# Performance work log

Measured on AMD Instinct MI355X. Metric: run time of the kernel, lower is better.

Reference implementation:

```python
import jax, jax.numpy as jnp
import numpy as np

N_QUBITS = 12
N_LAYERS = 4
BATCH = 4096
DIM = 2 ** N_QUBITS  # 4096


def _apply_1q(state, U, q):
    """Apply 2x2 complex gate U to qubit q. state: (B,) + (2,)*n, wire 0 = MSB (axis q+1)."""
    state = jnp.moveaxis(state, q + 1, -1)
    state = state @ U.T
    return jnp.moveaxis(state, -1, q + 1)


def _apply_cnot(state, c, t):
    """CNOT with control c, target t: flip target amplitudes where control bit == 1."""
    flipped = jnp.flip(state, axis=t + 1)
    shape = [2 if i == c + 1 else 1 for i in range(state.ndim)]
    ctrl = jnp.arange(2).reshape(shape)
    return jnp.where(ctrl == 1, flipped, state)


def setup_inputs() -> dict:
    key = jax.random.key(0)
    k1, k2 = jax.random.split(key)
    x = jax.random.normal(k1, (BATCH, DIM), dtype=jnp.float32)
    weights = jax.random.normal(k2, (N_LAYERS, N_QUBITS, 2), dtype=jnp.float32) * 0.1
    return {"x": x, "weights": weights}


def reference(x, weights):
    n, L = N_QUBITS, N_LAYERS
    B = x.shape[0]
    # AmplitudeEmbedding with normalize=True
    norm = jnp.linalg.norm(x, axis=-1, keepdims=True)
    state = (x / norm).astype(jnp.complex64).reshape((B,) + (2,) * n)
    for layer in range(L):
        for q in range(n):
            ty = weights[layer, q, 0]
            tz = weights[layer, q, 1]
            c, s = jnp.cos(ty / 2), jnp.sin(ty / 2)
            em = jnp.exp(-0.5j * tz.astype(jnp.complex64))  # e^{-i tz/2}
            ep = jnp.exp(+0.5j * tz.astype(jnp.complex64))
            # U = RZ(tz) @ RY(ty), fused single 2x2 gate per qubit
            U = jnp.stack([
                jnp.stack([c * em, -s * em]),
                jnp.stack([s * ep, c * ep]),
            ]).astype(jnp.complex64)
            state = _apply_1q(state, U, q)
        for q in range(n - 1):
            state = _apply_cnot(state, q, q + 1)
        if n > 2:
            state = _apply_cnot(state, n - 1, 0)
    probs = jnp.abs(state) ** 2  # (B,) + (2,)*n, float32
    reduce_axes = tuple(range(1, probs.ndim))
    outs = []
    for q in range(n):
        shape = [2 if i == q + 1 else 1 for i in range(probs.ndim)]
        sign = jnp.array([1.0, -1.0], dtype=probs.dtype).reshape(shape)
        outs.append(jnp.sum(probs * sign, axis=reduce_axes))
    return jnp.stack(outs, axis=-1)  # (B, n_qubits) <Z_q> expvals
```

## Files before the change

kernel.cpp:

```cpp
#include <hip/hip_runtime.h>

#define NQ   12
#define DIM  4096
#define NL   4
#define BLK  256

typedef unsigned short u16;
typedef unsigned int   u32;

struct L12 { u16 b[NQ]; };

static constexpr u32 lap(const L12& A, u32 x){ u32 r=0; for(int p=0;p<NQ;++p) if((x>>p)&1u) r^=A.b[p]; return r; }
static constexpr L12 lcomp(const L12& A, const L12& B){ L12 r{}; for(int p=0;p<NQ;++p) r.b[p]=(u16)lap(A,(u32)B.b[p]); return r; }
static constexpr L12 lident(){ L12 r{}; for(int p=0;p<NQ;++p) r.b[p]=(u16)(1u<<p); return r; }

static constexpr u32 applyT(u32 i){
  i ^= ((i>>0)&1u) << 11;
  for(int q=10;q>=0;--q){ int pc=11-q, pt=10-q; i ^= ((i>>pc)&1u) << pt; }
  return i;
}
static constexpr L12 lT(){ L12 t{}; for(int p=0;p<NQ;++p) t.b[p]=(u16)applyT(1u<<p); return t; }

static constexpr L12 linv(const L12& A){
  u16 v[NQ]; u16 u[NQ];
  for(int p=0;p<NQ;++p){ v[p]=A.b[p]; u[p]=(u16)(1u<<p); }
  for(int t=0;t<NQ;++t){
    int p=t; while(!((v[p]>>t)&1u)) ++p;
    u16 tv=v[p]; v[p]=v[t]; v[t]=tv; u16 tu=u[p]; u[p]=u[t]; u[t]=tu;
    for(int k=0;k<NQ;++k) if(k!=t && ((v[k]>>t)&1u)){ v[k]^=v[t]; u[k]^=u[t]; }
  }
  L12 r{}; for(int p=0;p<NQ;++p) r.b[p]=u[p]; return r;
}
static constexpr L12 ltr(const L12& A){
  L12 r{}; for(int p=0;p<NQ;++p) for(int q=0;q<NQ;++q) if((A.b[p]>>q)&1u) r.b[q]=(u16)(r.b[q]|(1u<<p));
  return r;
}

struct Tables {
  u16 cm[12][16];
  u16 wg[12][4];
  u16 sp[12][4];
  u16 wexp[NQ];
};

static constexpr Tables make_tables(){
  Tables tb{};
  const L12 T   = lT();
  const L12 Tit = ltr(linv(T));
  L12 A = lident();
  L12 W = lident();
  for(int l=0;l<NL;++l){
    for(int g=0;g<3;++g){
      const int st = l*3+g;
      u16 mm[4]={0,0,0,0};
      for(int i=0;i<4;++i){ mm[i]=A.b[4*g+i]; tb.wg[st][i]=W.b[4*g+i]; }
      u32 ech[4]={0,0,0,0}; int piv[4]={0,0,0,0};
      for(int i=0;i<4;++i){
        u32 v=mm[i];
        for(int k=0;k<i;++k) if((v>>piv[k])&1u) v^=ech[k];
        int t2=11; while(!((v>>t2)&1u)) --t2;
        piv[i]=t2; ech[i]=v;
      }
      for(int a2=0;a2<4;++a2) for(int b2=a2+1;b2<4;++b2)
        if(piv[b2]<piv[a2]){ int tt=piv[a2]; piv[a2]=piv[b2]; piv[b2]=tt; }
      for(int i=0;i<4;++i) tb.sp[st][i]=(u16)piv[i];
      for(int c=0;c<16;++c){ u32 m=0; for(int i=0;i<4;++i) if((c>>i)&1) m^=mm[i]; tb.cm[st][c]=(u16)m; }
    }
    A = lcomp(A, T);
    W = lcomp(W, Tit);
  }
  for(int p=0;p<NQ;++p) tb.wexp[p]=W.b[p];
  return tb;
}

__device__ constexpr Tables TB = make_tables();

static constexpr u16 UIMG[12] = {1,2,4,8, 3,5,6,7, 9,10,11,13};

static constexpr u32 swz(u32 j){
  u32 f=0;
  for(int k=4;k<12;++k) if((j>>k)&1u) f ^= (u32)UIMG[k];
  return j ^ (f & 15u);
}

struct Derived {
  u32 lane_c[12][8];
  u32 smb[12][4];
  u32 scmb[12][16];
  u32 eps[16];
  u32 tidc[8];
  u16 esgn[12];
};

static constexpr Derived make_derived(){
  const Tables tb = make_tables();
  Derived d{};
  for(int st=0; st<12; ++st){
    bool isp[12]={false,false,false,false,false,false,false,false,false,false,false,false};
    for(int i=0;i<4;++i) isp[tb.sp[st][i]]=true;
    int np[8]; int nn=0;
    for(int p=0;p<12;++p) if(!isp[p]) np[nn++]=p;
    int best=-1;
    for(int ms=0; ms<256; ++ms){
      int pc=0; for(int k=0;k<8;++k) pc+=(ms>>k)&1;
      if(pc!=6) continue;
      u16 bas[4]={0,0,0,0}; int r=0;
      for(int k=0;k<8;++k){
        if(!((ms>>k)&1)) continue;
        u16 x=(u16)(UIMG[np[k]]&15);
        while(x){
          int hb=3; while(!((x>>hb)&1)) --hb;
          if(bas[hb]) x=(u16)(x^bas[hb]);
          else { bas[hb]=x; ++r; x=0; }
        }
      }
      if(r==4){ best=ms; break; }
    }
    if(best<0) best=0x3F;
    int pos[8]; int lo=0, hi=6;
    for(int k=0;k<8;++k){ if((best>>k)&1) pos[lo++]=np[k]; else pos[hi++]=np[k]; }
    for(int k=0;k<8;++k){
      const u32 addr = swz(1u<<pos[k])<<3;
      u32 nib=0;
      for(int i=0;i<4;++i) nib |= (u32)((tb.wg[st][i]>>pos[k])&1u)<<i;
      d.lane_c[st][k] = addr | (nib<<28);
    }
    for(int i=0;i<4;++i)  d.smb[st][i]  = swz((u32)tb.cm[st][1<<i])<<3;
    for(int c=0;c<16;++c) d.scmb[st][c] = swz((u32)tb.cm[st][c])<<3;
  }
  for(int s=0;s<16;++s) d.eps[s]  = swz((u32)s<<8)<<3;
  for(int k=0;k<8;++k)  d.tidc[k] = swz(1u<<k)<<3;
  for(int q=0;q<12;++q){
    u16 m=0;
    for(int s=0;s<16;++s){
      int par=0; u32 v=((u32)s<<8) & (u32)tb.wexp[11-q];
      while(v){ par ^= (int)(v&1u); v>>=1; }
      m |= (u16)(par<<s);
    }
    d.esgn[q]=m;
  }
  return d;
}

__device__ constexpr Derived DV = make_derived();

__device__ __forceinline__ u32 step_base(int st, int tid){
  u32 acc=0;
#pragma unroll
  for(int k=0;k<8;++k) acc ^= DV.lane_c[st][k] & (0u-((u32)(tid>>k)&1u));
  const u32 nib = acc>>28;
  u32 b = acc & 0x0FFFFFFFu;
#pragma unroll
  for(int i=0;i<4;++i) b ^= DV.smb[st][i] & (0u-((nib>>i)&1u));
  return b;
}

template<bool WITHW, bool FIRST>
__device__ __forceinline__ void do_step(int st, int tid, char* lds, const float4* gq){
  const u32 base = step_base(st, tid);
  u32 ad[16]; float ar[16], ai[16];
#pragma unroll
  for(int c=0;c<16;++c){
    ad[c] = base ^ DV.scmb[st][c];
    if(FIRST){ ar[c] = *(const float*)(lds + ad[c]); ai[c]=0.f; }
    else { const float2 v = *(const float2*)(lds + ad[c]); ar[c]=v.x; ai[c]=v.y; }
  }
#pragma unroll
  for(int i=0;i<4;++i){
    const float4 g = gq[st*4+i];
#pragma unroll
    for(int c=0;c<16;++c){
      if((c>>i)&1) continue;
      const int c1 = c | (1<<i);
      const float a0r=ar[c], a0i=ai[c], a1r=ar[c1], a1i=ai[c1];
      const float t0r = fmaf(g.x,a0r, -(g.y*a1r));
      const float t0i = fmaf(g.x,a0i, -(g.y*a1i));
      const float t1r = fmaf(g.y,a0r,  g.x*a1r);
      const float t1i = fmaf(g.y,a0i,  g.x*a1i);
      ar[c]=t0r; ai[c]=t0i;
      if(WITHW){
        ar[c1] = fmaf(g.z,t1r, -(g.w*t1i));
        ai[c1] = fmaf(g.z,t1i,  g.w*t1r);
      } else { ar[c1]=t1r; ai[c1]=t1i; }
    }
  }
#pragma unroll
  for(int c=0;c<16;++c){ float2 v; v.x=ar[c]; v.y=ai[c]; *(float2*)(lds+ad[c]) = v; }
  __syncthreads();
}

__global__ __launch_bounds__(BLK) void qsim_kernel(const float* __restrict__ x,
                                                   const float* __restrict__ w,
                                                   float* __restrict__ out)
{
  __shared__ float2 st2[DIM];
  __shared__ float4 gq[NL*NQ];
  __shared__ float  wred[4][13];
  char* lds = (char*)st2;
  const int tid = threadIdx.x;
  const int bb  = blockIdx.x;

  if (tid < NL*NQ) {
    const int l = tid/NQ, p = tid%NQ, q = (NQ-1)-p;
    const float ty = w[(l*NQ+q)*2+0];
    const float tz = w[(l*NQ+q)*2+1];
    float sy,cy,szf,czf;
    sincosf(0.5f*ty, &sy, &cy);
    sincosf(tz, &szf, &czf);
    gq[tid] = make_float4(cy, sy, czf, szf);
  }

  u32 be=0;
#pragma unroll
  for(int k=0;k<8;++k) be ^= DV.tidc[k] & (0u-((u32)(tid>>k)&1u));

  const float* xr = x + (size_t)bb * DIM;
  float xv[16];
#pragma unroll
  for(int s=0;s<16;++s) xv[s] = xr[(s<<8)|tid];
#pragma unroll
  for(int s=0;s<16;++s) *(float*)(lds + (be ^ DV.eps[s])) = xv[s];
  __syncthreads();

  do_step<true,true>(0, tid, lds, gq);
#pragma unroll 1
  for(int st=1; st<9; ++st) do_step<true,false>(st, tid, lds, gq);
#pragma unroll 1
  for(int st=9; st<12; ++st) do_step<false,false>(st, tid, lds, gq);

  float pr[16]; float nrm=0.f;
#pragma unroll
  for(int s=0;s<16;++s){
    const float2 v = *(const float2*)(lds + (be ^ DV.eps[s]));
    pr[s] = fmaf(v.x,v.x, v.y*v.y);
    nrm += pr[s];
  }
  float accq[12];
#pragma unroll
  for(int q=0;q<12;++q){
    float a=0.f;
#pragma unroll
    for(int s=0;s<16;++s){
      if((DV.esgn[q]>>s)&1) a -= pr[s]; else a += pr[s];
    }
    const u32 b = ((u32)__popc((u32)tid & (u32)TB.wexp[11-q]) & 1u) << 31;
    accq[q] = __uint_as_float(__float_as_uint(a) ^ b);
  }
#pragma unroll
  for(int o=32;o;o>>=1){
    nrm += __shfl_xor(nrm,o);
#pragma unroll
    for(int q=0;q<12;++q) accq[q] += __shfl_xor(accq[q],o);
  }
  const int wid = tid>>6;
  if((tid&63)==0){
#pragma unroll
    for(int q=0;q<12;++q) wred[wid][q]=accq[q];
    wred[wid][12]=nrm;
  }
  __syncthreads();
  if(tid<NQ){
    const float s0 = wred[0][tid]+wred[1][tid]+wred[2][tid]+wred[3][tid];
    const float sn = wred[0][12]+wred[1][12]+wred[2][12]+wred[3][12];
    out[(size_t)bb*NQ + tid] = s0/sn;
  }
}

extern "C" void kernel_launch(void* const* d_in, const int* in_sizes, int n_in,
                              void* d_out, int out_size, void* d_ws, size_t ws_size,
                              hipStream_t stream) {
  const float* x = (const float*)d_in[0];
  const float* w = (const float*)d_in[1];
  float* out = (float*)d_out;
  const int B = in_sizes[0] / DIM;
  qsim_kernel<<<B, BLK, 0, stream>>>(x, w, out);
}
```

Before: 130.2 us.

## Fuse first/last gate stages with global load and reduction, use shear rotations

The initial global load now reads each thread's 16 amplitudes directly in the layout the first gate stage needs, so stage 0 runs before the first LDS store and the separate staging pass goes away. The final stage is fused with the expectation reduction, removing one LDS write/read round trip and a barrier. Rotations are rewritten as three-shear (tan/sin) FMA sequences to cut arithmetic, gate parameters move to a one-block prep kernel in workspace, and the stage loop is fully unrolled with a 4-blocks-per-CU launch bound. The trade-offs are an extra kernel launch, possible precision differences from the tan-based shear form, and more register pressure from unrolling.

```diff
diff --git a/kernel.cpp b/kernel.cpp
--- a/kernel.cpp
+++ b/kernel.cpp
@@ -35,6 +35,7 @@
   L12 r{}; for(int p=0;p<NQ;++p) for(int q=0;q<NQ;++q) if((A.b[p]>>q)&1u) r.b[q]=(u16)(r.b[q]|(1u<<p));
   return r;
 }
+static constexpr int cpop(u32 v){ int n=0; while(v){ n+=(int)(v&1u); v>>=1; } return n; }
 
 struct Tables {
   u16 cm[12][16];
@@ -87,9 +88,11 @@
   u32 lane_c[12][8];
   u32 smb[12][4];
   u32 scmb[12][16];
-  u32 eps[16];
-  u32 tidc[8];
-  u16 esgn[12];
+  u32 g0lane[8];
+  u32 u11lane[8];
+  u32 u11smb[4];
+  u16 csgn[12];
+  u16 pm[12];
 };
 
 static constexpr Derived make_derived(){
@@ -124,145 +127,174 @@
       u32 nib=0;
       for(int i=0;i<4;++i) nib |= (u32)((tb.wg[st][i]>>pos[k])&1u)<<i;
       d.lane_c[st][k] = addr | (nib<<28);
+      if(st==0)  d.g0lane[k]  = 1u<<pos[k];
+      if(st==11) d.u11lane[k] = 1u<<pos[k];
     }
     for(int i=0;i<4;++i)  d.smb[st][i]  = swz((u32)tb.cm[st][1<<i])<<3;
     for(int c=0;c<16;++c) d.scmb[st][c] = swz((u32)tb.cm[st][c])<<3;
-  }
-  for(int s=0;s<16;++s) d.eps[s]  = swz((u32)s<<8)<<3;
-  for(int k=0;k<8;++k)  d.tidc[k] = swz(1u<<k)<<3;
+    if(st==11) for(int i=0;i<4;++i) d.u11smb[i] = (u32)tb.cm[11][1<<i];
+  }
   for(int q=0;q<12;++q){
+    d.pm[q] = tb.wexp[11-q];
     u16 m=0;
-    for(int s=0;s<16;++s){
-      int par=0; u32 v=((u32)s<<8) & (u32)tb.wexp[11-q];
-      while(v){ par ^= (int)(v&1u); v>>=1; }
-      m |= (u16)(par<<s);
-    }
-    d.esgn[q]=m;
+    for(int c=0;c<16;++c){
+      const int par = cpop((u32)tb.cm[11][c] & (u32)tb.wexp[11-q]) & 1;
+      m |= (u16)(par<<c);
+    }
+    d.csgn[q]=m;
   }
   return d;
 }
 
 __device__ constexpr Derived DV = make_derived();
 
-__device__ __forceinline__ u32 step_base(int st, int tid){
-  u32 acc=0;
-#pragma unroll
-  for(int k=0;k<8;++k) acc ^= DV.lane_c[st][k] & (0u-((u32)(tid>>k)&1u));
-  const u32 nib = acc>>28;
-  u32 b = acc & 0x0FFFFFFFu;
-#pragma unroll
-  for(int i=0;i<4;++i) b ^= DV.smb[st][i] & (0u-((nib>>i)&1u));
-  return b;
-}
-
-template<bool WITHW, bool FIRST>
-__device__ __forceinline__ void do_step(int st, int tid, char* lds, const float4* gq){
-  const u32 base = step_base(st, tid);
-  u32 ad[16]; float ar[16], ai[16];
-#pragma unroll
-  for(int c=0;c<16;++c){
-    ad[c] = base ^ DV.scmb[st][c];
-    if(FIRST){ ar[c] = *(const float*)(lds + ad[c]); ai[c]=0.f; }
-    else { const float2 v = *(const float2*)(lds + ad[c]); ar[c]=v.x; ai[c]=v.y; }
-  }
+template<int ST, bool WITHW>
+__device__ __forceinline__ void gates(float (&ar)[16], float (&ai)[16], const float4* __restrict__ gw){
 #pragma unroll
   for(int i=0;i<4;++i){
-    const float4 g = gq[st*4+i];
+    const float4 g = gw[ST*4+i];
 #pragma unroll
     for(int c=0;c<16;++c){
       if((c>>i)&1) continue;
-      const int c1 = c | (1<<i);
-      const float a0r=ar[c], a0i=ai[c], a1r=ar[c1], a1i=ai[c1];
-      const float t0r = fmaf(g.x,a0r, -(g.y*a1r));
-      const float t0i = fmaf(g.x,a0i, -(g.y*a1i));
-      const float t1r = fmaf(g.y,a0r,  g.x*a1r);
-      const float t1i = fmaf(g.y,a0i,  g.x*a1i);
-      ar[c]=t0r; ai[c]=t0i;
+      const int c1 = c|(1<<i);
+      float ur = fmaf(-g.x, ar[c1], ar[c]);
+      float ui = fmaf(-g.x, ai[c1], ai[c]);
+      float vr = fmaf( g.y, ur, ar[c1]);
+      float vi = fmaf( g.y, ui, ai[c1]);
+      ar[c] = fmaf(-g.x, vr, ur);
+      ai[c] = fmaf(-g.x, vi, ui);
       if(WITHW){
-        ar[c1] = fmaf(g.z,t1r, -(g.w*t1i));
-        ai[c1] = fmaf(g.z,t1i,  g.w*t1r);
-      } else { ar[c1]=t1r; ai[c1]=t1i; }
-    }
-  }
-#pragma unroll
-  for(int c=0;c<16;++c){ float2 v; v.x=ar[c]; v.y=ai[c]; *(float2*)(lds+ad[c]) = v; }
+        const float t = fmaf(-g.z, vi, vr);
+        vi = fmaf( g.w, t, vi);
+        vr = fmaf(-g.z, vi, t);
+      }
+      ar[c1]=vr; ai[c1]=vi;
+    }
+  }
+}
+
+template<int ST, bool WITHW>
+__device__ __forceinline__ void mid_step(const u32* msk, char* lds, const float4* __restrict__ gw){
+  u32 acc=0;
+#pragma unroll
+  for(int k=0;k<8;++k) acc ^= DV.lane_c[ST][k]&msk[k];
+  const u32 nib = acc>>28;
+  u32 base = acc & 0x0FFFFFFFu;
+#pragma unroll
+  for(int i=0;i<4;++i) base ^= DV.smb[ST][i] & (0u-((nib>>i)&1u));
+  u32 ad[16]; float ar[16], ai[16];
+#pragma unroll
+  for(int c=0;c<16;++c){
+    ad[c] = base ^ DV.scmb[ST][c];
+    const float2 v = *(const float2*)(lds+ad[c]);
+    ar[c]=v.x; ai[c]=v.y;
+  }
+  gates<ST,WITHW>(ar,ai,gw);
+#pragma unroll
+  for(int c=0;c<16;++c){ float2 v; v.x=ar[c]; v.y=ai[c]; *(float2*)(lds+ad[c])=v; }
   __syncthreads();
 }
 
-__global__ __launch_bounds__(BLK) void qsim_kernel(const float* __restrict__ x,
-                                                   const float* __restrict__ w,
-                                                   float* __restrict__ out)
+__global__ void prep_kernel(const float* __restrict__ w, float4* __restrict__ gw){
+  const int t = threadIdx.x;
+  if(t < NL*NQ){
+    const int l=t/NQ, p=t%NQ, q=(NQ-1)-p;
+    const float ty=w[(l*NQ+q)*2+0], tz=w[(l*NQ+q)*2+1];
+    gw[t]=make_float4(tanf(0.25f*ty), sinf(0.5f*ty), tanf(0.5f*tz), sinf(tz));
+  }
+}
+
+__global__ __launch_bounds__(BLK, 4) void qsim_kernel(const float* __restrict__ x,
+                                                      const float4* __restrict__ gw,
+                                                      float* __restrict__ out)
 {
   __shared__ float2 st2[DIM];
-  __shared__ float4 gq[NL*NQ];
   __shared__ float  wred[4][13];
   char* lds = (char*)st2;
   const int tid = threadIdx.x;
   const int bb  = blockIdx.x;
 
-  if (tid < NL*NQ) {
-    const int l = tid/NQ, p = tid%NQ, q = (NQ-1)-p;
-    const float ty = w[(l*NQ+q)*2+0];
-    const float tz = w[(l*NQ+q)*2+1];
-    float sy,cy,szf,czf;
-    sincosf(0.5f*ty, &sy, &cy);
-    sincosf(tz, &szf, &czf);
-    gq[tid] = make_float4(cy, sy, czf, szf);
-  }
-
-  u32 be=0;
-#pragma unroll
-  for(int k=0;k<8;++k) be ^= DV.tidc[k] & (0u-((u32)(tid>>k)&1u));
-
-  const float* xr = x + (size_t)bb * DIM;
-  float xv[16];
-#pragma unroll
-  for(int s=0;s<16;++s) xv[s] = xr[(s<<8)|tid];
-#pragma unroll
-  for(int s=0;s<16;++s) *(float*)(lds + (be ^ DV.eps[s])) = xv[s];
+  u32 msk[8];
+#pragma unroll
+  for(int k=0;k<8;++k) msk[k]=0u-((u32)(tid>>k)&1u);
+
+  u32 rep0=0, acc0=0;
+#pragma unroll
+  for(int k=0;k<8;++k){ rep0 ^= DV.g0lane[k]&msk[k]; acc0 ^= DV.lane_c[0][k]&msk[k]; }
+  const u32 base0 = acc0 & 0x0FFFFFFFu;
+
+  float ar[16], ai[16];
+  const float* xr = x + (size_t)bb*DIM + rep0;
+#pragma unroll
+  for(int s=0;s<4;++s){
+    const float4 v = *reinterpret_cast<const float4*>(xr + 4*s);
+    ar[4*s+0]=v.x; ar[4*s+1]=v.y; ar[4*s+2]=v.z; ar[4*s+3]=v.w;
+    ai[4*s+0]=0.f; ai[4*s+1]=0.f; ai[4*s+2]=0.f; ai[4*s+3]=0.f;
+  }
+  gates<0,true>(ar,ai,gw);
+#pragma unroll
+  for(int c=0;c<16;++c){ float2 v; v.x=ar[c]; v.y=ai[c];
+    *(float2*)(lds + (base0 ^ DV.scmb[0][c])) = v; }
   __syncthreads();
 
-  do_step<true,true>(0, tid, lds, gq);
-#pragma unroll 1
-  for(int st=1; st<9; ++st) do_step<true,false>(st, tid, lds, gq);
-#pragma unroll 1
-  for(int st=9; st<12; ++st) do_step<false,false>(st, tid, lds, gq);
-
-  float pr[16]; float nrm=0.f;
-#pragma unroll
-  for(int s=0;s<16;++s){
-    const float2 v = *(const float2*)(lds + (be ^ DV.eps[s]));
-    pr[s] = fmaf(v.x,v.x, v.y*v.y);
-    nrm += pr[s];
-  }
-  float accq[12];
-#pragma unroll
-  for(int q=0;q<12;++q){
-    float a=0.f;
-#pragma unroll
-    for(int s=0;s<16;++s){
-      if((DV.esgn[q]>>s)&1) a -= pr[s]; else a += pr[s];
-    }
-    const u32 b = ((u32)__popc((u32)tid & (u32)TB.wexp[11-q]) & 1u) << 31;
-    accq[q] = __uint_as_float(__float_as_uint(a) ^ b);
-  }
-#pragma unroll
-  for(int o=32;o;o>>=1){
-    nrm += __shfl_xor(nrm,o);
-#pragma unroll
-    for(int q=0;q<12;++q) accq[q] += __shfl_xor(accq[q],o);
-  }
-  const int wid = tid>>6;
-  if((tid&63)==0){
-#pragma unroll
-    for(int q=0;q<12;++q) wred[wid][q]=accq[q];
-    wred[wid][12]=nrm;
-  }
-  __syncthreads();
-  if(tid<NQ){
-    const float s0 = wred[0][tid]+wred[1][tid]+wred[2][tid]+wred[3][tid];
-    const float sn = wred[0][12]+wred[1][12]+wred[2][12]+wred[3][12];
-    out[(size_t)bb*NQ + tid] = s0/sn;
+  mid_step<1,true >(msk,lds,gw);
+  mid_step<2,true >(msk,lds,gw);
+  mid_step<3,true >(msk,lds,gw);
+  mid_step<4,true >(msk,lds,gw);
+  mid_step<5,true >(msk,lds,gw);
+  mid_step<6,true >(msk,lds,gw);
+  mid_step<7,true >(msk,lds,gw);
+  mid_step<8,true >(msk,lds,gw);
+  mid_step<9,false>(msk,lds,gw);
+  mid_step<10,false>(msk,lds,gw);
+
+  {
+    u32 acc=0, urep=0;
+#pragma unroll
+    for(int k=0;k<8;++k){ acc ^= DV.lane_c[11][k]&msk[k]; urep ^= DV.u11lane[k]&msk[k]; }
+    const u32 nib = acc>>28;
+    u32 base = acc & 0x0FFFFFFFu;
+#pragma unroll
+    for(int i=0;i<4;++i){ const u32 mi=0u-((nib>>i)&1u); base ^= DV.smb[11][i]&mi; urep ^= DV.u11smb[i]&mi; }
+#pragma unroll
+    for(int c=0;c<16;++c){
+      const float2 v = *(const float2*)(lds + (base ^ DV.scmb[11][c]));
+      ar[c]=v.x; ai[c]=v.y;
+    }
+    gates<11,false>(ar,ai,gw);
+
+    float pr[16]; float nrm=0.f;
+#pragma unroll
+    for(int c=0;c<16;++c) pr[c]=fmaf(ar[c],ar[c], ai[c]*ai[c]);
+#pragma unroll
+    for(int c=0;c<16;++c) nrm += pr[c];
+    float accq[12];
+#pragma unroll
+    for(int q=0;q<12;++q){
+      float a=0.f;
+#pragma unroll
+      for(int c=0;c<16;++c){ if((DV.csgn[q]>>c)&1) a-=pr[c]; else a+=pr[c]; }
+      const u32 sb = ((u32)__popc(urep & (u32)DV.pm[q]) & 1u)<<31;
+      accq[q]=__uint_as_float(__float_as_uint(a)^sb);
+    }
+#pragma unroll
+    for(int o=32;o;o>>=1){
+      nrm += __shfl_xor(nrm,o);
+#pragma unroll
+      for(int q=0;q<12;++q) accq[q]+=__shfl_xor(accq[q],o);
+    }
+    const int wid=tid>>6;
+    if((tid&63)==0){
+#pragma unroll
+      for(int q=0;q<12;++q) wred[wid][q]=accq[q];
+      wred[wid][12]=nrm;
+    }
+    __syncthreads();
+    if(tid<NQ){
+      const float s0=wred[0][tid]+wred[1][tid]+wred[2][tid]+wred[3][tid];
+      const float sn=wred[0][12]+wred[1][12]+wred[2][12]+wred[3][12];
+      out[(size_t)bb*NQ+tid]=s0/sn;
+    }
   }
 }
 
@@ -272,6 +304,8 @@
   const float* x = (const float*)d_in[0];
   const float* w = (const float*)d_in[1];
   float* out = (float*)d_out;
+  float4* gw = (float4*)d_ws;
   const int B = in_sizes[0] / DIM;
-  qsim_kernel<<<B, BLK, 0, stream>>>(x, w, out);
-}
+  prep_kernel<<<1, 64, 0, stream>>>(w, gw);
+  qsim_kernel<<<B, BLK, 0, stream>>>(x, gw, out);
+}
```

Result: faster. 112.7 us (-13.4%).
